# Kernel tuning notes

Hardware: AMD Instinct MI355X
Metric: run time of the kernel (lower is better)

## Reference

```python
import jax, jax.numpy as jnp
import numpy as np
from jax import lax

# Module constants (from init_kwargs)
B, C = 2, 64            # batch, in_channel
H, W, D = 64, 64, 64    # size
GROUPS = 2


def setup_inputs() -> dict:
    key = jax.random.key(0)
    ks = jax.random.split(key, 4)
    x = jax.random.normal(ks[0], (B, H * W * D, C), dtype=jnp.float32)
    # TransverseConv: Conv3d(2, W*2, (H,3,3), pad (0,1,1)) -> weight (O,I,kD,kH,kW)
    w_t = jax.random.normal(ks[1], (W * GROUPS, GROUPS, H, 3, 3), dtype=jnp.float32) * 0.02
    b_t = jnp.zeros((W * GROUPS,), jnp.float32)
    # CoronalConv: Conv3d(2, W*2, (3,3,D), pad (1,1,0))
    w_c = jax.random.normal(ks[2], (W * GROUPS, GROUPS, 3, 3, D), dtype=jnp.float32) * 0.02
    b_c = jnp.zeros((W * GROUPS,), jnp.float32)
    # map: Conv3d(2C, C, 1) stored as dense (C, 2C)
    w_map = jax.random.normal(ks[3], (C, 2 * C), dtype=jnp.float32) * 0.02
    b_map = jnp.zeros((C,), jnp.float32)
    return {"x": x, "w_t": w_t, "b_t": b_t, "w_c": w_c, "b_c": b_c,
            "w_map": w_map, "b_map": b_map}


def _forward(x, w_t, b_t, w_c, b_c, w_map, b_map):
    Bx, N, Cx = x.shape
    xg = x.transpose(0, 2, 1).reshape(Bx, Cx, H, W, D)   # (B,C,H,W,D)
    shortcut = xg
    xr = xg.reshape(Bx * Cx // GROUPS, GROUPS, H, W, D)
    dn = ('NCDHW', 'OIDHW', 'NCDHW')
    # Transverse: kernel spans full H -> output (B*C/2, 2W, 1, W, D)
    tans = lax.conv_general_dilated(xr, w_t, (1, 1, 1), [(0, 0), (1, 1), (1, 1)],
                                    dimension_numbers=dn)
    tans = tans + b_t[None, :, None, None, None]
    tans = tans.reshape(Bx, Cx, W, W, D)                 # (B,C,W,W,D)
    # Coronal: kernel spans full D -> output (B*C/2, 2W, H, W, 1)
    cor = lax.conv_general_dilated(xr, w_c, (1, 1, 1), [(1, 1), (1, 1), (0, 0)],
                                   dimension_numbers=dn)
    cor = cor + b_c[None, :, None, None, None]
    cor = cor.reshape(Bx, Cx, W, H, W)                   # (B,C,W,H,W)
    t1 = tans.transpose(0, 1, 3, 2, 4)                   # (B,C,W,W,D)
    c1 = cor.transpose(0, 1, 4, 3, 2)                    # (B,C,W,H,W)
    f = jnp.matmul(c1, t1).transpose(0, 1, 3, 2, 4)      # (B,C,H,W,D)
    attn = jnp.matmul(cor, tans).transpose(0, 1, 3, 2, 4)  # (B,C,H,W,D)
    cat = jnp.concatenate([shortcut * f, attn], axis=1)  # (B,2C,H,W,D)
    mapped = jnp.einsum('bkhwd,ck->bchwd', cat, w_map) + b_map[None, :, None, None, None]
    out = jax.nn.gelu(mapped, approximate=False)         # torch nn.GELU = exact erf
    return out.reshape(Bx, Cx, -1).transpose(0, 2, 1)    # (B,N,C)


def reference(x, w_t, b_t, w_c, b_c, w_map, b_map):
    return _forward(x, w_t, b_t, w_c, b_c, w_map, b_map)
```

## Files before the change

### kernel.cpp

```cpp
#include <hip/hip_runtime.h>
#include <hip/hip_bf16.h>
#include <math.h>

#define HWD 262144

typedef __attribute__((ext_vector_type(8))) short bf16x8;
typedef __attribute__((ext_vector_type(16))) float f32x16;

__device__ inline unsigned short bfu(float f) {
    __hip_bfloat16 h = __float2bfloat16(f);
    return *reinterpret_cast<unsigned short*>(&h);
}

__global__ void k_prep(const float* __restrict__ w_t, const float* __restrict__ w_c,
                       const float* __restrict__ w_map,
                       __hip_bfloat16* __restrict__ A_t, __hip_bfloat16* __restrict__ A_c,
                       __hip_bfloat16* __restrict__ Wb) {
    int i = blockIdx.x * 256 + threadIdx.x;
    if (i < 147456) {
        int kk = i & 15, oc = (i >> 4) & 127, ks = i >> 11;
        int z4 = ks & 3, kq = ks >> 2;
        int g = kq / 9, tap = kq - 9 * g;
        int z = z4 * 16 + kk;
        A_t[i] = __float2bfloat16(w_t[((oc * 2 + g) * 64 + z) * 9 + tap]);
        A_c[i] = __float2bfloat16(w_c[((oc * 2 + g) * 9 + tap) * 64 + z]);
    }
    if (i < 8192) {
        Wb[i] = __float2bfloat16(w_map[i]);
    }
}

__device__ inline void pack_row_bf16(__hip_bfloat16* dst, const float* src) {
    unsigned short u[16];
#pragma unroll
    for (int j = 0; j < 16; ++j) u[j] = bfu(src[j]);
    uint4* q = reinterpret_cast<uint4*>(dst);
    q[0] = *reinterpret_cast<const uint4*>(&u[0]);
    q[1] = *reinterpret_cast<const uint4*>(&u[8]);
}

__global__ void k_trans_c(const float* __restrict__ x, __hip_bfloat16* __restrict__ Xc) {
    __shared__ unsigned short tile[256][68];
    int b = blockIdx.y;
    long n0 = (long)blockIdx.x * 256;
    int t = threadIdx.x;
    const float4* xp4 = (const float4*)(x + ((long)b * HWD + n0) * 64);
#pragma unroll
    for (int i = 0; i < 16; ++i) {
        int f4i = i * 256 + t;
        float4 v = xp4[f4i];
        int nl = f4i >> 4, c4 = (f4i & 15) * 4;
        ushort4 u;
        u.x = bfu(v.x); u.y = bfu(v.y); u.z = bfu(v.z); u.w = bfu(v.w);
        *(ushort4*)&tile[nl][c4] = u;
    }
    __syncthreads();
    int c = t >> 2, hwl = t & 3;
    int hw0 = blockIdx.x * 4;
    __hip_bfloat16* dst0 = Xc + (long)(b * 64 + c) * HWD + (long)(hw0 + hwl) * 16;
#pragma unroll
    for (int z4 = 0; z4 < 4; ++z4) {
        unsigned short u[16];
#pragma unroll
        for (int j = 0; j < 16; ++j) u[j] = tile[hwl * 64 + z4 * 16 + j][c];
        __hip_bfloat16* dst = dst0 + z4 * 65536;
        *(uint4*)dst = *(const uint4*)&u[0];
        *(uint4*)(dst + 8) = *(const uint4*)&u[8];
    }
}

__global__ void k_trans_t(const float* __restrict__ x, __hip_bfloat16* __restrict__ Xt) {
    __shared__ unsigned short tile[256][68];
    int b = blockIdx.y;
    int wd0 = blockIdx.x * 4;
    int t = threadIdx.x;
    const float* xb = x + (long)b * HWD * 64 + (long)wd0 * 64;
#pragma unroll
    for (int i = 0; i < 16; ++i) {
        int idx = i * 256 + t;
        int h = idx >> 6, f = idx & 63;
        float4 v = *(const float4*)(xb + (long)h * 262144 + f * 4);
        int wdl = f >> 4, c4 = (f & 15) * 4;
        ushort4 u;
        u.x = bfu(v.x); u.y = bfu(v.y); u.z = bfu(v.z); u.w = bfu(v.w);
        *(ushort4*)&tile[wdl * 64 + h][c4] = u;
    }
    __syncthreads();
    int c = t >> 2, wdl = t & 3;
    __hip_bfloat16* dst0 = Xt + (long)(b * 64 + c) * HWD + (long)(wd0 + wdl) * 16;
#pragma unroll
    for (int z4 = 0; z4 < 4; ++z4) {
        unsigned short u[16];
#pragma unroll
        for (int j = 0; j < 16; ++j) u[j] = tile[wdl * 64 + z4 * 16 + j][c];
        __hip_bfloat16* dst = dst0 + z4 * 65536;
        *(uint4*)dst = *(const uint4*)&u[0];
        *(uint4*)(dst + 8) = *(const uint4*)&u[8];
    }
}

__global__ __launch_bounds__(256, 3) void k_conv_mfma(
        const __hip_bfloat16* __restrict__ X, const __hip_bfloat16* __restrict__ Aglob,
        const float* __restrict__ bias, float* __restrict__ Out) {
    int L = blockIdx.x;
    int grp = (L & 7) * 8 + ((L >> 3) >> 5);
    int pt = (L >> 3) & 31;
    int b = grp >> 5, ch = grp & 31;
    int p0 = pt * 2;
    const short* Xg = (const short*)(X + ((long)(b * 64 + 2 * ch)) * HWD);
    const short* Ag = (const short*)Aglob;
    int t = threadIdx.x;
    int lane = t & 63, wv = t >> 6;
    int O0 = (wv >> 1) * 64;
    int N0 = (wv & 1) * 64;
    int lrow = lane & 31, lq = lane >> 5;

    __shared__ __align__(16) short Bsm[2][4][2][1024];

    f32x16 acc00 = {0}, acc01 = {0}, acc10 = {0}, acc11 = {0};

    int srow = t >> 1, shalf = t & 1;
    int spr = srow >> 6, sq = srow & 63;
    const uint4 zero4 = {0u, 0u, 0u, 0u};
    uint4 ld0, ld1, ld2, ld3;

    auto stage_load = [&](int kq) {
        int g = (kq >= 9) ? 1 : 0;
        int tap = kq - 9 * g;
        int r = tap / 3, s = tap - 3 * r;
        int pp = p0 + spr + r - 1, qq = sq + s - 1;
        bool ok = ((unsigned)pp < 64u) && ((unsigned)qq < 64u);
        const short* px = Xg + (long)g * HWD + (pp * 64 + qq) * 16 + shalf * 8;
        ld0 = ok ? *(const uint4*)(px)           : zero4;
        ld1 = ok ? *(const uint4*)(px + 65536)   : zero4;
        ld2 = ok ? *(const uint4*)(px + 131072)  : zero4;
        ld3 = ok ? *(const uint4*)(px + 196608)  : zero4;
    };
    auto stage_write = [&](int buf) {
        *(uint4*)&Bsm[buf][0][shalf][srow * 8] = ld0;
        *(uint4*)&Bsm[buf][1][shalf][srow * 8] = ld1;
        *(uint4*)&Bsm[buf][2][shalf][srow * 8] = ld2;
        *(uint4*)&Bsm[buf][3][shalf][srow * 8] = ld3;
    };

    stage_load(0);
    stage_write(0);
    __syncthreads();

    int buf = 0;
    for (int kq = 0; kq < 18; ++kq) {
        if (kq < 17) stage_load(kq + 1);
#pragma unroll
        for (int z4 = 0; z4 < 4; ++z4) {
            int ks = kq * 4 + z4;
            const short* Apk = Ag + ks * 2048 + (O0 + lrow) * 16 + lq * 8;
            uint4 a0u = *(const uint4*)(Apk);
            uint4 a1u = *(const uint4*)(Apk + 512);
            bf16x8 a0 = *(bf16x8*)&a0u;
            bf16x8 a1 = *(bf16x8*)&a1u;
            bf16x8 b0 = *(const bf16x8*)&Bsm[buf][z4][lq][(N0 + lrow) * 8];
            bf16x8 b1 = *(const bf16x8*)&Bsm[buf][z4][lq][(N0 + 32 + lrow) * 8];
            acc00 = __builtin_amdgcn_mfma_f32_32x32x16_bf16(a0, b0, acc00, 0, 0, 0);
            acc01 = __builtin_amdgcn_mfma_f32_32x32x16_bf16(a0, b1, acc01, 0, 0, 0);
            acc10 = __builtin_amdgcn_mfma_f32_32x32x16_bf16(a1, b0, acc10, 0, 0, 0);
            acc11 = __builtin_amdgcn_mfma_f32_32x32x16_bf16(a1, b1, acc11, 0, 0, 0);
        }
        if (kq < 17) {
            stage_write(buf ^ 1);
            __syncthreads();
            buf ^= 1;
        }
    }

    long base0 = ((long)(b * 64 + 2 * ch)) * HWD + (long)p0 * 64;
    int n0l = N0 + lrow, n1l = N0 + 32 + lrow;
    long noff0 = (long)(n0l >> 6) * 64 + (n0l & 63);
    long noff1 = (long)(n1l >> 6) * 64 + (n1l & 63);
#pragma unroll
    for (int reg = 0; reg < 16; ++reg) {
        int row = (reg & 3) + 8 * (reg >> 2) + 4 * lq;
        int oc0 = O0 + row, oc1 = O0 + 32 + row;
        long cb0 = base0 + (long)(oc0 >> 6) * HWD + (long)(oc0 & 63) * 4096;
        long cb1 = base0 + (long)(oc1 >> 6) * HWD + (long)(oc1 & 63) * 4096;
        float bs0 = bias[oc0], bs1 = bias[oc1];
        Out[cb0 + noff0] = acc00[reg] + bs0;
        Out[cb0 + noff1] = acc01[reg] + bs0;
        Out[cb1 + noff0] = acc10[reg] + bs1;
        Out[cb1 + noff1] = acc11[reg] + bs1;
    }
}

__global__ __launch_bounds__(128) void k_attn(const float* __restrict__ Cc,
        const float* __restrict__ T, __hip_bfloat16* __restrict__ At) {
    __shared__ float As[64][65];
    __shared__ float Bs[64][64];
    int bc = blockIdx.x >> 6, w2 = blockIdx.x & 63;
    const float4* Ap4 = (const float4*)(Cc + ((long)bc * 64 + w2) * 4096);
    const float4* Bp4 = (const float4*)(T + ((long)bc * 64 + w2) * 4096);
    int t = threadIdx.x;
#pragma unroll
    for (int i = 0; i < 8; ++i) {
        int f = i * 128 + t;
        int r = f >> 4, q4 = (f & 15) * 4;
        float4 v = Ap4[f];
        As[r][q4 + 0] = v.x; As[r][q4 + 1] = v.y; As[r][q4 + 2] = v.z; As[r][q4 + 3] = v.w;
        float4 w = Bp4[f];
        *(float4*)&Bs[r][q4] = w;
    }
    __syncthreads();
    int h2 = t >> 2, dg = (t & 3) * 16;
    f32x16 acc0 = {0}, acc1 = {0};
    for (int k = 0; k < 64; ++k) {
        float a0 = As[h2][k];
        float a1 = As[h2 + 32][k];
        const float* br = &Bs[k][dg];
#pragma unroll
        for (int i = 0; i < 16; ++i) {
            acc0[i] = fmaf(a0, br[i], acc0[i]);
            acc1[i] = fmaf(a1, br[i], acc1[i]);
        }
    }
    float tmp[16];
    __hip_bfloat16* Ab = At + (long)bc * HWD + (long)h2 * 4096 + w2 * 64 + dg;
#pragma unroll
    for (int i = 0; i < 16; ++i) tmp[i] = acc0[i];
    pack_row_bf16(Ab, tmp);
#pragma unroll
    for (int i = 0; i < 16; ++i) tmp[i] = acc1[i];
    pack_row_bf16(Ab + 32L * 4096, tmp);
}

__global__ __launch_bounds__(256, 2) void k_f(const float* __restrict__ Cc,
        const float* __restrict__ T, __hip_bfloat16* __restrict__ F) {
    __shared__ float As[16][64][8];
    __shared__ float Bs[16][8][68];
    int L = blockIdx.x;
    int xcd = L & 7, j = L >> 3;
    int bc = xcd * 16 + (j >> 3), wt = j & 7;
    const float* Ab = Cc + (long)bc * HWD + wt * 8;
    const float* Bb = T + (long)bc * HWD + wt * 8 * 64;
    int t = threadIdx.x;
    int w = t & 7, h2 = t >> 3;
    f32x16 p00 = {0}, p01 = {0}, p02 = {0}, p03 = {0};
    f32x16 p10 = {0}, p11 = {0}, p12 = {0}, p13 = {0};

    for (int w2c = 0; w2c < 4; ++w2c) {
        __syncthreads();
#pragma unroll
        for (int i = 0; i < 8; ++i) {
            int f = i * 256 + t;
            int half = f & 1, hh = (f >> 1) & 63, kk = f >> 7;
            float4 v = *(const float4*)(Ab + (long)(w2c * 16 + kk) * 4096 + hh * 64 + half * 4);
            *(float4*)&As[kk][hh][half * 4] = v;
        }
#pragma unroll
        for (int i = 0; i < 8; ++i) {
            int f = i * 256 + t;
            int d4 = f & 15, ww = (f >> 4) & 7, kk = f >> 7;
            float4 v = *(const float4*)(Bb + (long)(w2c * 16 + kk) * 4096 + ww * 64 + d4 * 4);
            *(float4*)&Bs[kk][ww][d4 * 4] = v;
        }
        __syncthreads();
        for (int kk = 0; kk < 16; ++kk) {
            float a0 = As[kk][h2][w];
            float a1 = As[kk][h2 + 32][w];
            const float* br = &Bs[kk][w][0];
#pragma unroll
            for (int i = 0; i < 16; ++i) {
                p00[i] = fmaf(a0, br[i], p00[i]);
                p01[i] = fmaf(a0, br[16 + i], p01[i]);
                p02[i] = fmaf(a0, br[32 + i], p02[i]);
                p03[i] = fmaf(a0, br[48 + i], p03[i]);
                p10[i] = fmaf(a1, br[i], p10[i]);
                p11[i] = fmaf(a1, br[16 + i], p11[i]);
                p12[i] = fmaf(a1, br[32 + i], p12[i]);
                p13[i] = fmaf(a1, br[48 + i], p13[i]);
            }
        }
    }
    __hip_bfloat16* Fp = F + (long)bc * HWD + (long)h2 * 4096 + (wt * 8 + w) * 64;
    float tmp[16];
#pragma unroll
    for (int i = 0; i < 16; ++i) tmp[i] = p00[i];
    pack_row_bf16(Fp, tmp);
#pragma unroll
    for (int i = 0; i < 16; ++i) tmp[i] = p01[i];
    pack_row_bf16(Fp + 16, tmp);
#pragma unroll
    for (int i = 0; i < 16; ++i) tmp[i] = p02[i];
    pack_row_bf16(Fp + 32, tmp);
#pragma unroll
    for (int i = 0; i < 16; ++i) tmp[i] = p03[i];
    pack_row_bf16(Fp + 48, tmp);
    __hip_bfloat16* Fq = Fp + 32L * 4096;
#pragma unroll
    for (int i = 0; i < 16; ++i) tmp[i] = p10[i];
    pack_row_bf16(Fq, tmp);
#pragma unroll
    for (int i = 0; i < 16; ++i) tmp[i] = p11[i];
    pack_row_bf16(Fq + 16, tmp);
#pragma unroll
    for (int i = 0; i < 16; ++i) tmp[i] = p12[i];
    pack_row_bf16(Fq + 32, tmp);
#pragma unroll
    for (int i = 0; i < 16; ++i) tmp[i] = p13[i];
    pack_row_bf16(Fq + 48, tmp);
}

__global__ __launch_bounds__(256, 2) void k_map(const float* __restrict__ x,
        const __hip_bfloat16* __restrict__ F, const __hip_bfloat16* __restrict__ At,
        const __hip_bfloat16* __restrict__ Wb, const float* __restrict__ b_map,
        float* __restrict__ out) {
    __shared__ float xs[16][257];
    __shared__ __hip_bfloat16 fa[16][264];

    int t = threadIdx.x;
    long n0 = (long)blockIdx.x * 256;
    int b = (int)(n0 >> 18);
    long nn0 = n0 & (HWD - 1);
    const float* xblk = x + n0 * 64;
    const __hip_bfloat16* Fb = F + (long)b * 64 * HWD + nn0;
    const __hip_bfloat16* Ab = At + (long)b * 64 * HWD + nn0;

    int lane = t & 63, wv = t >> 6;
    int lrow = lane & 31, lhalf = lane >> 5;

    const short* Wp = (const short*)Wb;
    bf16x8 wb0[8], wb1[8];
#pragma unroll
    for (int kc = 0; kc < 8; ++kc) {
        uint4 u0 = *(const uint4*)(Wp + lrow * 128 + kc * 16 + lhalf * 8);
        uint4 u1 = *(const uint4*)(Wp + (32 + lrow) * 128 + kc * 16 + lhalf * 8);
        wb0[kc] = *(bf16x8*)&u0;
        wb1[kc] = *(bf16x8*)&u1;
    }

    f32x16 acc00 = {0}, acc01 = {0}, acc10 = {0}, acc11 = {0};

#pragma unroll
    for (int kc = 0; kc < 8; ++kc) {
        __syncthreads();
        if (kc < 4) {
#pragma unroll
            for (int i2 = 0; i2 < 4; ++i2) {
                int f = i2 * 256 + t;
                int nr = f >> 2, j4 = (f & 3) * 4;
                float4 v = *(const float4*)(xblk + nr * 64 + kc * 16 + j4);
                xs[j4 + 0][nr] = v.x;
                xs[j4 + 1][nr] = v.y;
                xs[j4 + 2][nr] = v.z;
                xs[j4 + 3][nr] = v.w;
            }
#pragma unroll
            for (int it = 0; it < 2; ++it) {
                int idx = it * 256 + t;
                int row = idx >> 5, seg = idx & 31;
                *(uint4*)&fa[row][seg * 8] =
                    *(const uint4*)(Fb + (long)(kc * 16 + row) * HWD + seg * 8);
            }
        } else {
#pragma unroll
            for (int it = 0; it < 2; ++it) {
                int idx = it * 256 + t;
                int row = idx >> 5, seg = idx & 31;
                *(uint4*)&fa[row][seg * 8] =
                    *(const uint4*)(Ab + (long)((kc - 4) * 16 + row) * HWD + seg * 8);
            }
        }
        __syncthreads();
        unsigned short pv[16];
        if (kc < 4) {
#pragma unroll
            for (int k2 = 0; k2 < 16; ++k2) {
                float p = xs[k2][t] * __bfloat162float(fa[k2][t]);
                pv[k2] = bfu(p);
            }
        } else {
#pragma unroll
            for (int k2 = 0; k2 < 16; ++k2)
                pv[k2] = *reinterpret_cast<const unsigned short*>(&fa[k2][t]);
        }
        unsigned lo0 = (unsigned)pv[0]  | ((unsigned)pv[1]  << 16);
        unsigned lo1 = (unsigned)pv[2]  | ((unsigned)pv[3]  << 16);
        unsigned lo2 = (unsigned)pv[4]  | ((unsigned)pv[5]  << 16);
        unsigned lo3 = (unsigned)pv[6]  | ((unsigned)pv[7]  << 16);
        unsigned hi0 = (unsigned)pv[8]  | ((unsigned)pv[9]  << 16);
        unsigned hi1 = (unsigned)pv[10] | ((unsigned)pv[11] << 16);
        unsigned hi2 = (unsigned)pv[12] | ((unsigned)pv[13] << 16);
        unsigned hi3 = (unsigned)pv[14] | ((unsigned)pv[15] << 16);
        int sl0 = lane & 31, sl1 = lane | 32;
        bool lowh = lane < 32;
        unsigned s00 = __shfl(hi0, sl0), s01 = __shfl(hi1, sl0);
        unsigned s02 = __shfl(hi2, sl0), s03 = __shfl(hi3, sl0);
        unsigned r00 = __shfl(lo0, sl1), r01 = __shfl(lo1, sl1);
        unsigned r02 = __shfl(lo2, sl1), r03 = __shfl(lo3, sl1);
        uint4 ua0, ua1;
        ua0.x = lowh ? lo0 : s00; ua0.y = lowh ? lo1 : s01;
        ua0.z = lowh ? lo2 : s02; ua0.w = lowh ? lo3 : s03;
        ua1.x = lowh ? r00 : hi0; ua1.y = lowh ? r01 : hi1;
        ua1.z = lowh ? r02 : hi2; ua1.w = lowh ? r03 : hi3;
        bf16x8 a0 = *(bf16x8*)&ua0;
        bf16x8 a1 = *(bf16x8*)&ua1;
        acc00 = __builtin_amdgcn_mfma_f32_32x32x16_bf16(a0, wb0[kc], acc00, 0, 0, 0);
        acc01 = __builtin_amdgcn_mfma_f32_32x32x16_bf16(a0, wb1[kc], acc01, 0, 0, 0);
        acc10 = __builtin_amdgcn_mfma_f32_32x32x16_bf16(a1, wb0[kc], acc10, 0, 0, 0);
        acc11 = __builtin_amdgcn_mfma_f32_32x32x16_bf16(a1, wb1[kc], acc11, 0, 0, 0);
    }

    float bs0 = b_map[lrow];
    float bs1 = b_map[32 + lrow];
    const float inv_sqrt2 = 0.70710678118654752440f;
    float* ob = out + (n0 + wv * 64) * 64;
#pragma unroll
    for (int reg = 0; reg < 16; ++reg) {
        int nrow = (reg & 3) + 8 * (reg >> 2) + 4 * lhalf;
        float v00 = acc00[reg] + bs0;
        float v01 = acc01[reg] + bs1;
        float v10 = acc10[reg] + bs0;
        float v11 = acc11[reg] + bs1;
        v00 = 0.5f * v00 * (1.f + erff(v00 * inv_sqrt2));
        v01 = 0.5f * v01 * (1.f + erff(v01 * inv_sqrt2));
        v10 = 0.5f * v10 * (1.f + erff(v10 * inv_sqrt2));
        v11 = 0.5f * v11 * (1.f + erff(v11 * inv_sqrt2));
        ob[(long)nrow * 64 + lrow] = v00;
        ob[(long)nrow * 64 + 32 + lrow] = v01;
        ob[(long)(32 + nrow) * 64 + lrow] = v10;
        ob[(long)(32 + nrow) * 64 + 32 + lrow] = v11;
    }
}

extern "C" void kernel_launch(void* const* d_in, const int* in_sizes, int n_in,
                              void* d_out, int out_size, void* d_ws, size_t ws_size,
                              hipStream_t stream) {
    const float* x     = (const float*)d_in[0];
    const float* w_t   = (const float*)d_in[1];
    const float* b_t   = (const float*)d_in[2];
    const float* w_c   = (const float*)d_in[3];
    const float* b_c   = (const float*)d_in[4];
    const float* w_map = (const float*)d_in[5];
    const float* b_map = (const float*)d_in[6];
    float* out = (float*)d_out;
    float* ws = (float*)d_ws;

    __hip_bfloat16* Xc = (__hip_bfloat16*)ws;
    __hip_bfloat16* Xt = (__hip_bfloat16*)(ws + 16777216L);
    float* T = ws + 33554432L;
    float* Cc = out;
    __hip_bfloat16* A_t = (__hip_bfloat16*)(ws + 67108864L);
    __hip_bfloat16* A_c = (__hip_bfloat16*)(ws + 67182592L);
    __hip_bfloat16* Wb = (__hip_bfloat16*)(ws + 67256320L);
    __hip_bfloat16* At_bf = Xc;
    __hip_bfloat16* F_bf = Xt;

    hipLaunchKernelGGL(k_prep, dim3(576), dim3(256), 0, stream, w_t, w_c, w_map, A_t, A_c, Wb);
    hipLaunchKernelGGL(k_trans_c, dim3(1024, 2), dim3(256), 0, stream, x, Xc);
    hipLaunchKernelGGL(k_trans_t, dim3(1024, 2), dim3(256), 0, stream, x, Xt);
    hipLaunchKernelGGL(k_conv_mfma, dim3(2048), dim3(256), 0, stream, Xt, A_t, b_t, T);
    hipLaunchKernelGGL(k_conv_mfma, dim3(2048), dim3(256), 0, stream, Xc, A_c, b_c, Cc);
    hipLaunchKernelGGL(k_attn, dim3(8192), dim3(128), 0, stream, Cc, T, At_bf);
    hipLaunchKernelGGL(k_f, dim3(1024), dim3(256), 0, stream, Cc, T, F_bf);
    hipLaunchKernelGGL(k_map, dim3(2048), dim3(256), 0, stream, x, F_bf, At_bf, Wb, b_map, out);
}
```

Baseline: 762.6 us.

## Double-buffer k_map shared-memory tiles with register prefetch of next chunk

```diff
diff --git a/kernel.cpp b/kernel.cpp
--- a/kernel.cpp
+++ b/kernel.cpp
@@ -307,12 +307,12 @@
     pack_row_bf16(Fq + 48, tmp);
 }
 
-__global__ __launch_bounds__(256, 2) void k_map(const float* __restrict__ x,
+__global__ __launch_bounds__(256, 3) void k_map(const float* __restrict__ x,
         const __hip_bfloat16* __restrict__ F, const __hip_bfloat16* __restrict__ At,
         const __hip_bfloat16* __restrict__ Wb, const float* __restrict__ b_map,
         float* __restrict__ out) {
-    __shared__ float xs[16][257];
-    __shared__ __hip_bfloat16 fa[16][264];
+    __shared__ float xs[2][16][257];
+    __shared__ __hip_bfloat16 fa[2][16][264];
 
     int t = threadIdx.x;
     long n0 = (long)blockIdx.x * 256;
@@ -337,48 +337,67 @@
 
     f32x16 acc00 = {0}, acc01 = {0}, acc10 = {0}, acc11 = {0};
 
+    float4 xa, xb_, xc_, xd;
+    uint4 fe, ff;
+    int nrA = t >> 2, j4A = (t & 3) * 4;
+    int rowF0 = t >> 5, segF0 = t & 31;
+    int rowF1 = (256 + t) >> 5, segF1 = t & 31;
+
+    auto load_chunk = [&](int kc) {
+        if (kc < 4) {
+            xa  = *(const float4*)(xblk + (nrA +   0) * 64 + kc * 16 + j4A);
+            xb_ = *(const float4*)(xblk + (nrA +  64) * 64 + kc * 16 + j4A);
+            xc_ = *(const float4*)(xblk + (nrA + 128) * 64 + kc * 16 + j4A);
+            xd  = *(const float4*)(xblk + (nrA + 192) * 64 + kc * 16 + j4A);
+            fe = *(const uint4*)(Fb + (long)(kc * 16 + rowF0) * HWD + segF0 * 8);
+            ff = *(const uint4*)(Fb + (long)(kc * 16 + rowF1) * HWD + segF1 * 8);
+        } else {
+            fe = *(const uint4*)(Ab + (long)((kc - 4) * 16 + rowF0) * HWD + segF0 * 8);
+            ff = *(const uint4*)(Ab + (long)((kc - 4) * 16 + rowF1) * HWD + segF1 * 8);
+        }
+    };
+    auto write_chunk = [&](int kc, int buf) {
+        if (kc < 4) {
+            xs[buf][j4A + 0][nrA +   0] = xa.x;
+            xs[buf][j4A + 1][nrA +   0] = xa.y;
+            xs[buf][j4A + 2][nrA +   0] = xa.z;
+            xs[buf][j4A + 3][nrA +   0] = xa.w;
+            xs[buf][j4A + 0][nrA +  64] = xb_.x;
+            xs[buf][j4A + 1][nrA +  64] = xb_.y;
+            xs[buf][j4A + 2][nrA +  64] = xb_.z;
+            xs[buf][j4A + 3][nrA +  64] = xb_.w;
+            xs[buf][j4A + 0][nrA + 128] = xc_.x;
+            xs[buf][j4A + 1][nrA + 128] = xc_.y;
+            xs[buf][j4A + 2][nrA + 128] = xc_.z;
+            xs[buf][j4A + 3][nrA + 128] = xc_.w;
+            xs[buf][j4A + 0][nrA + 192] = xd.x;
+            xs[buf][j4A + 1][nrA + 192] = xd.y;
+            xs[buf][j4A + 2][nrA + 192] = xd.z;
+            xs[buf][j4A + 3][nrA + 192] = xd.w;
+        }
+        *(uint4*)&fa[buf][rowF0][segF0 * 8] = fe;
+        *(uint4*)&fa[buf][rowF1][segF1 * 8] = ff;
+    };
+
+    load_chunk(0);
+    write_chunk(0, 0);
+    __syncthreads();
+
 #pragma unroll
     for (int kc = 0; kc < 8; ++kc) {
-        __syncthreads();
-        if (kc < 4) {
-#pragma unroll
-            for (int i2 = 0; i2 < 4; ++i2) {
-                int f = i2 * 256 + t;
-                int nr = f >> 2, j4 = (f & 3) * 4;
-                float4 v = *(const float4*)(xblk + nr * 64 + kc * 16 + j4);
-                xs[j4 + 0][nr] = v.x;
-                xs[j4 + 1][nr] = v.y;
-                xs[j4 + 2][nr] = v.z;
-                xs[j4 + 3][nr] = v.w;
-            }
-#pragma unroll
-            for (int it = 0; it < 2; ++it) {
-                int idx = it * 256 + t;
-                int row = idx >> 5, seg = idx & 31;
-                *(uint4*)&fa[row][seg * 8] =
-                    *(const uint4*)(Fb + (long)(kc * 16 + row) * HWD + seg * 8);
-            }
-        } else {
-#pragma unroll
-            for (int it = 0; it < 2; ++it) {
-                int idx = it * 256 + t;
-                int row = idx >> 5, seg = idx & 31;
-                *(uint4*)&fa[row][seg * 8] =
-                    *(const uint4*)(Ab + (long)((kc - 4) * 16 + row) * HWD + seg * 8);
-            }
-        }
-        __syncthreads();
+        int buf = kc & 1;
+        if (kc < 7) load_chunk(kc + 1);
         unsigned short pv[16];
         if (kc < 4) {
 #pragma unroll
             for (int k2 = 0; k2 < 16; ++k2) {
-                float p = xs[k2][t] * __bfloat162float(fa[k2][t]);
+                float p = xs[buf][k2][t] * __bfloat162float(fa[buf][k2][t]);
                 pv[k2] = bfu(p);
             }
         } else {
 #pragma unroll
             for (int k2 = 0; k2 < 16; ++k2)
-                pv[k2] = *reinterpret_cast<const unsigned short*>(&fa[k2][t]);
+                pv[k2] = *reinterpret_cast<const unsigned short*>(&fa[buf][k2][t]);
         }
         unsigned lo0 = (unsigned)pv[0]  | ((unsigned)pv[1]  << 16);
         unsigned lo1 = (unsigned)pv[2]  | ((unsigned)pv[3]  << 16);
@@ -405,6 +424,10 @@
         acc01 = __builtin_amdgcn_mfma_f32_32x32x16_bf16(a0, wb1[kc], acc01, 0, 0, 0);
         acc10 = __builtin_amdgcn_mfma_f32_32x32x16_bf16(a1, wb0[kc], acc10, 0, 0, 0);
         acc11 = __builtin_amdgcn_mfma_f32_32x32x16_bf16(a1, wb1[kc], acc11, 0, 0, 0);
+        if (kc < 7) {
+            write_chunk(kc + 1, buf ^ 1);
+            __syncthreads();
+        }
     }
 
     float bs0 = b_map[lrow];
```

Result: no change. 757.1 us (-0.7%).
